# Kernel optimization log

Measured on AMD Instinct MI355X. Metric: run time of the kernel, lower is better.

## Reference

```python
import jax, jax.numpy as jnp
import numpy as np

B, S, HID = 1, 2048, 4096
N_HEADS, N_KV, HEAD_DIM = 32, 8, 128
N_REP = N_HEADS // N_KV
ROPE_THETA = 10000.0
NEG_INF = -1e9


def setup_inputs() -> dict:
    key = jax.random.key(0)
    ks = jax.random.split(key, 5)
    hidden_states = jax.random.normal(ks[0], (B, S, HID), dtype=jnp.float32)
    Wq = jax.random.normal(ks[1], (HID, N_HEADS * HEAD_DIM), dtype=jnp.float32) * 0.02
    Wk = jax.random.normal(ks[2], (HID, N_KV * HEAD_DIM), dtype=jnp.float32) * 0.02
    Wv = jax.random.normal(ks[3], (HID, N_KV * HEAD_DIM), dtype=jnp.float32) * 0.02
    Wo = jax.random.normal(ks[4], (N_HEADS * HEAD_DIM, HID), dtype=jnp.float32) * 0.02
    # causal additive mask [B, 1, S, S]
    causal = jnp.tril(jnp.ones((S, S), dtype=bool))
    attention_mask = jnp.where(causal, 0.0, NEG_INF).astype(jnp.float32)[None, None]
    position_ids = jnp.broadcast_to(jnp.arange(S, dtype=jnp.int32)[None], (B, S))
    return {
        "hidden_states": hidden_states, "Wq": Wq, "Wk": Wk, "Wv": Wv, "Wo": Wo,
        "attention_mask": attention_mask, "position_ids": position_ids,
    }


def _rotate_half(x):
    half = x.shape[-1] // 2
    return jnp.concatenate([-x[..., half:], x[..., :half]], axis=-1)


def _rope_tables(position_ids):
    # inv_freq: [head_dim/2]
    inv_freq = 1.0 / (ROPE_THETA ** (jnp.arange(0, HEAD_DIM, 2, dtype=jnp.float32) / HEAD_DIM))
    # freqs: [B, S, head_dim/2]
    freqs = position_ids.astype(jnp.float32)[..., None] * inv_freq
    emb = jnp.concatenate([freqs, freqs], axis=-1)  # [B, S, head_dim]
    # [B, 1, S, head_dim] to broadcast over heads
    return jnp.cos(emb)[:, None], jnp.sin(emb)[:, None]


def reference(hidden_states, Wq, Wk, Wv, Wo, attention_mask, position_ids):
    b, s, _ = hidden_states.shape
    # projections -> [B, H, S, D]
    q = (hidden_states @ Wq).reshape(b, s, N_HEADS, HEAD_DIM).transpose(0, 2, 1, 3)
    k = (hidden_states @ Wk).reshape(b, s, N_KV, HEAD_DIM).transpose(0, 2, 1, 3)
    v = (hidden_states @ Wv).reshape(b, s, N_KV, HEAD_DIM).transpose(0, 2, 1, 3)
    cos, sin = _rope_tables(position_ids)
    q = q * cos + _rotate_half(q) * sin
    k = k * cos + _rotate_half(k) * sin
    # GQA repeat_kv (repeat_interleave over head dim)
    k = jnp.repeat(k, N_REP, axis=1)
    v = jnp.repeat(v, N_REP, axis=1)
    scores = jnp.einsum("bhqd,bhkd->bhqk", q, k) / jnp.sqrt(jnp.float32(HEAD_DIM))
    scores = scores + attention_mask
    probs = jax.nn.softmax(scores.astype(jnp.float32), axis=-1).astype(q.dtype)
    attn = jnp.einsum("bhqk,bhkd->bhqd", probs, v)
    attn = attn.transpose(0, 2, 1, 3).reshape(b, s, N_HEADS * HEAD_DIM)
    return attn @ Wo
```

## Files before the change

kernel.cpp:

```cpp
#include <hip/hip_runtime.h>
#include <hip/hip_bf16.h>

#define S_LEN 2048
#define HIDDEN 4096
#define NH 32
#define NKV 8
#define HD 128
#define NQKV 6144

typedef __bf16 bf16_t;
typedef __bf16 bf16x8 __attribute__((ext_vector_type(8)));
typedef __bf16 bf16x4 __attribute__((ext_vector_type(4)));
typedef float f32x4 __attribute__((ext_vector_type(4)));

typedef __attribute__((address_space(1))) void gvoid;
typedef __attribute__((address_space(3))) void lvoid;

__device__ __forceinline__ void gload_lds16(const void* g, void* l) {
    __builtin_amdgcn_global_load_lds((gvoid*)g, (lvoid*)l, 16, 0, 0);
}

__device__ __forceinline__ float fast_exp2(float x) {
    return __builtin_amdgcn_exp2f(x);
}

__global__ void cast_bf16_kernel(const float* __restrict__ in, bf16_t* __restrict__ out, int n4) {
    int stride = gridDim.x * blockDim.x;
    for (int idx = blockIdx.x * blockDim.x + threadIdx.x; idx < n4; idx += stride) {
        float4 v = ((const float4*)in)[idx];
        bf16x4 o;
        o.x = (bf16_t)v.x; o.y = (bf16_t)v.y; o.z = (bf16_t)v.z; o.w = (bf16_t)v.w;
        ((bf16x4*)out)[idx] = o;
    }
}

__global__ __launch_bounds__(256) void transpose_cast_kernel(const float* __restrict__ in,
                                                             bf16_t* __restrict__ out,
                                                             int ldin, int ldout) {
    __shared__ float t[32][33];
    int c0 = blockIdx.x * 32, r0 = blockIdx.y * 32;
    int tx = threadIdx.x, ty = threadIdx.y;
#pragma unroll
    for (int i = 0; i < 4; ++i)
        t[ty + i * 8][tx] = in[(size_t)(r0 + ty + i * 8) * ldin + c0 + tx];
    __syncthreads();
#pragma unroll
    for (int i = 0; i < 4; ++i)
        out[(size_t)(c0 + ty + i * 8) * ldout + r0 + tx] = (bf16_t)t[tx][ty + i * 8];
}

__global__ __launch_bounds__(256) void transpose_bf16_kernel(const bf16_t* __restrict__ in,
                                                             bf16_t* __restrict__ out,
                                                             int ldin, int ldout) {
    __shared__ float t[32][33];
    int c0 = blockIdx.x * 32, r0 = blockIdx.y * 32;
    int tx = threadIdx.x, ty = threadIdx.y;
#pragma unroll
    for (int i = 0; i < 4; ++i)
        t[ty + i * 8][tx] = (float)in[(size_t)(r0 + ty + i * 8) * ldin + c0 + tx];
    __syncthreads();
#pragma unroll
    for (int i = 0; i < 4; ++i)
        out[(size_t)(c0 + ty + i * 8) * ldout + r0 + tx] = (bf16_t)t[tx][ty + i * 8];
}

template<typename OutT>
__global__ __launch_bounds__(512, 2) void gemm_ring_kernel(const bf16_t* __restrict__ A,
                                                           const bf16_t* __restrict__ Bt,
                                                           OutT* __restrict__ C,
                                                           int M, int N, int K) {
    __shared__ bf16_t As[3][128 * 32];
    __shared__ bf16_t Bs[3][256 * 32];
    const int tid = threadIdx.x;
    const int lane = tid & 63, w = tid >> 6;
    const int wm = w >> 2, wn = w & 3;
    const int g = lane >> 4, c16 = lane & 15;
    const int srow = lane >> 2;
    const int scg = ((lane & 3) ^ ((lane >> 3) & 3)) * 8;
    const int rdc = (g ^ ((c16 >> 1) & 3)) * 8;

    const int nbm = M / 128;
    const int cpx = gridDim.x >> 3;
    const int bid = blockIdx.x;
    const int swz = (bid & 7) * cpx + (bid >> 3);
    const int bm = swz % nbm, bn = swz / nbm;

    const bf16_t* Ab = A + (size_t)(bm * 128) * K;
    const bf16_t* Bb = Bt + (size_t)(bn * 256) * K;

    auto stage = [&](int slot, int kt) {
        const bf16_t* Ak = Ab + (size_t)kt * 32;
        const bf16_t* Bk = Bb + (size_t)kt * 32;
        {
            int rb = 16 * w;
            gload_lds16(Ak + (size_t)(rb + srow) * K + scg, &As[slot][rb * 32]);
        }
#pragma unroll
        for (int j = 0; j < 2; ++j) {
            int rb = 32 * w + 16 * j;
            gload_lds16(Bk + (size_t)(rb + srow) * K + scg, &Bs[slot][rb * 32]);
        }
    };

    f32x4 acc[4][4];
#pragma unroll
    for (int i = 0; i < 4; ++i)
#pragma unroll
        for (int j = 0; j < 4; ++j)
            acc[i][j] = (f32x4){0.f, 0.f, 0.f, 0.f};

    const int NT = K / 32;
    stage(0, 0);
    stage(1, 1);

    int slot = 0, slot2 = 2;
    for (int t = 0; t < NT; ++t) {
        asm volatile("s_waitcnt vmcnt(3)" ::: "memory");
        __builtin_amdgcn_s_barrier();
        __builtin_amdgcn_sched_barrier(0);
        __builtin_amdgcn_s_setprio(1);

        bf16x8 af[4], bf[4];
#pragma unroll
        for (int i = 0; i < 4; ++i) {
            int arow = wm * 64 + i * 16 + c16;
            af[i] = *(const bf16x8*)&As[slot][arow * 32 + rdc];
            int brow = wn * 64 + i * 16 + c16;
            bf[i] = *(const bf16x8*)&Bs[slot][brow * 32 + rdc];
        }
        int nk = t + 2;
        if (nk >= NT) nk -= NT;
        stage(slot2, nk);

#pragma unroll
        for (int i = 0; i < 4; ++i)
#pragma unroll
            for (int j = 0; j < 4; ++j)
                acc[i][j] = __builtin_amdgcn_mfma_f32_16x16x32_bf16(af[i], bf[j], acc[i][j], 0, 0, 0);
        __builtin_amdgcn_s_setprio(0);

        slot = (slot + 1) % 3;
        slot2 = (slot2 + 1) % 3;
    }

#pragma unroll
    for (int mi = 0; mi < 4; ++mi)
#pragma unroll
        for (int ni = 0; ni < 4; ++ni) {
            int col = bn * 256 + wn * 64 + ni * 16 + c16;
#pragma unroll
            for (int r = 0; r < 4; ++r) {
                int row = bm * 128 + wm * 64 + mi * 16 + g * 4 + r;
                C[(size_t)row * N + col] = (OutT)acc[mi][ni][r];
            }
        }
}

__global__ void rope_kernel(const bf16_t* __restrict__ in, bf16_t* __restrict__ out,
                            const int* __restrict__ pos, int H, int ld, float scale) {
    int idx = blockIdx.x * blockDim.x + threadIdx.x;
    int total = S_LEN * H * 64;
    if (idx >= total) return;
    int d = idx & 63;
    int h = (idx >> 6) % H;
    int s = idx / (64 * H);
    const bf16_t* base = in + (size_t)s * ld + h * HD;
    float x0 = (float)base[d], x1 = (float)base[d + 64];
    float p = (float)pos[s];
    float invf = fast_exp2(-0.20762050593046935f * (float)d);
    float f = p * invf;
    float sn, cs;
    __sincosf(f, &sn, &cs);
    float o0 = (x0 * cs - x1 * sn) * scale;
    float o1 = (x1 * cs + x0 * sn) * scale;
    bf16_t* ob = out + ((size_t)h * S_LEN + s) * HD;
    ob[d] = (bf16_t)o0;
    ob[d + 64] = (bf16_t)o1;
}

#define PLD 68
__global__ __launch_bounds__(512) void attn_kernel(const bf16_t* __restrict__ Q,
                                                   const bf16_t* __restrict__ K,
                                                   const bf16_t* __restrict__ Vt,
                                                   bf16_t* __restrict__ O) {
    __shared__ bf16_t Ks[2][64 * 128];
    __shared__ bf16_t Vs[2][128 * 64];
    __shared__ bf16_t Pl[8][16 * PLD];
    const int tid = threadIdx.x;
    const int lane = tid & 63, w = tid >> 6;
    const int bid = blockIdx.x;
    const int h = bid & 31;
    const int x = bid >> 5;
    const int wg = w >> 2, wi = w & 3;
    const int qtile = wg == 0 ? x : 15 - x;
    const int qb = qtile * 128 + wi * 32;
    const int kv = h >> 2;
    const int g = lane >> 4, c16 = lane & 15;
    const int c7 = c16 & 7;
    const bf16_t* Qh = Q + (size_t)h * S_LEN * HD;
    const bf16_t* Kh = K + (size_t)kv * S_LEN * HD;
    const bf16_t* Vh = Vt + (size_t)kv * HD * S_LEN;
    bf16_t* P = Pl[w];

    auto stage = [&](int buf, int kb) {
        bf16_t* Kd = Ks[buf];
        bf16_t* Vd = Vs[buf];
#pragma unroll
        for (int j = 0; j < 2; ++j) {
            int i = w * 2 + j;
            {
                int row = 4 * i + (lane >> 4);
                int sc = (lane & 15) ^ (row & 7);
                gload_lds16(Kh + (size_t)(kb + row) * HD + sc * 8, Kd + i * 512);
            }
            {
                int row = 8 * i + (lane >> 3);
                int sc = (lane & 7) ^ ((lane >> 3) & 7);
                gload_lds16(Vh + (size_t)row * S_LEN + kb + sc * 8, Vd + i * 512);
            }
        }
    };

    bf16x8 qf[2][4];
#pragma unroll
    for (int rg = 0; rg < 2; ++rg)
#pragma unroll
        for (int c = 0; c < 4; ++c)
            qf[rg][c] = *(const bf16x8*)(Qh + (size_t)(qb + rg * 16 + c16) * HD + c * 32 + g * 8);

    bf16x8 ones;
#pragma unroll
    for (int j = 0; j < 8; ++j) ones[j] = (bf16_t)1.0f;

    f32x4 acc_o[2][8];
#pragma unroll
    for (int rg = 0; rg < 2; ++rg)
#pragma unroll
        for (int dt = 0; dt < 8; ++dt) acc_o[rg][dt] = (f32x4){0.f, 0.f, 0.f, 0.f};
    f32x4 acc_l[2] = {(f32x4){0.f, 0.f, 0.f, 0.f}, (f32x4){0.f, 0.f, 0.f, 0.f}};
    float m[2][4];
#pragma unroll
    for (int rg = 0; rg < 2; ++rg)
#pragma unroll
        for (int r = 0; r < 4; ++r) m[rg][r] = -1e30f;

    const int nkt = 32 - 2 * x;
    stage(0, 0);
    __syncthreads();
    int cur = 0;

    bf16x8 pf[2][2];
    for (int kt = 0; kt < nkt; ++kt) {
        if (kt + 1 < nkt) stage(cur ^ 1, (kt + 1) * 64);
        const int kb = kt * 64;
        const bf16_t* Kb = Ks[cur];
        const bf16_t* Vb = Vs[cur];

        if (kb <= qb + 31) {
            const bool diag = (kb + 63 > qb);

            f32x4 sacc[2][4];
#pragma unroll
            for (int rg = 0; rg < 2; ++rg)
#pragma unroll
                for (int t = 0; t < 4; ++t) sacc[rg][t] = (f32x4){0.f, 0.f, 0.f, 0.f};
#pragma unroll
            for (int t = 0; t < 4; ++t) {
                const bf16_t* krow = Kb + (t * 16 + c16) * 128;
#pragma unroll
                for (int cc = 0; cc < 4; ++cc) {
                    bf16x8 kf = *(const bf16x8*)(krow + (((cc * 4 + g) ^ c7) * 8));
                    sacc[0][t] = __builtin_amdgcn_mfma_f32_16x16x32_bf16(qf[0][cc], kf, sacc[0][t], 0, 0, 0);
                    sacc[1][t] = __builtin_amdgcn_mfma_f32_16x16x32_bf16(qf[1][cc], kf, sacc[1][t], 0, 0, 0);
                }
            }
#pragma unroll
            for (int rg = 0; rg < 2; ++rg) {
                float p[4][4], mxr[4];
#pragma unroll
                for (int r = 0; r < 4; ++r) {
                    int qq = qb + rg * 16 + g * 4 + r;
#pragma unroll
                    for (int t = 0; t < 4; ++t) {
                        float sv = sacc[rg][t][r];
                        if (diag && (kb + t * 16 + c16 > qq)) sv = -1e30f;
                        p[t][r] = sv;
                    }
                    float mx = fmaxf(fmaxf(p[0][r], p[1][r]), fmaxf(p[2][r], p[3][r]));
                    mx = fmaxf(mx, __shfl_xor(mx, 1));
                    mx = fmaxf(mx, __shfl_xor(mx, 2));
                    mx = fmaxf(mx, __shfl_xor(mx, 4));
                    mx = fmaxf(mx, __shfl_xor(mx, 8));
                    mxr[r] = mx;
                }
                bool resc = false;
#pragma unroll
                for (int r = 0; r < 4; ++r) resc = resc || (mxr[r] > m[rg][r] + 8.f);
                if (__any(resc)) {
#pragma unroll
                    for (int r = 0; r < 4; ++r) {
                        float mn = fmaxf(m[rg][r], mxr[r]);
                        float al = fast_exp2(m[rg][r] - mn);
                        m[rg][r] = mn;
                        acc_l[rg][r] *= al;
#pragma unroll
                        for (int dt = 0; dt < 8; ++dt) acc_o[rg][dt][r] *= al;
                    }
                }
#pragma unroll
                for (int r = 0; r < 4; ++r)
#pragma unroll
                    for (int t = 0; t < 4; ++t)
                        p[t][r] = fast_exp2(p[t][r] - m[rg][r]);
#pragma unroll
                for (int t = 0; t < 4; ++t)
#pragma unroll
                    for (int r = 0; r < 4; ++r)
                        P[(g * 4 + r) * PLD + t * 16 + c16] = (bf16_t)p[t][r];
                pf[rg][0] = *(const bf16x8*)(P + c16 * PLD + g * 8);
                pf[rg][1] = *(const bf16x8*)(P + c16 * PLD + 32 + g * 8);
            }
            acc_l[0] = __builtin_amdgcn_mfma_f32_16x16x32_bf16(pf[0][0], ones, acc_l[0], 0, 0, 0);
            acc_l[0] = __builtin_amdgcn_mfma_f32_16x16x32_bf16(pf[0][1], ones, acc_l[0], 0, 0, 0);
            acc_l[1] = __builtin_amdgcn_mfma_f32_16x16x32_bf16(pf[1][0], ones, acc_l[1], 0, 0, 0);
            acc_l[1] = __builtin_amdgcn_mfma_f32_16x16x32_bf16(pf[1][1], ones, acc_l[1], 0, 0, 0);
#pragma unroll
            for (int dt = 0; dt < 8; ++dt) {
                const bf16_t* vrow = Vb + (dt * 16 + c16) * 64;
                bf16x8 vf0 = *(const bf16x8*)(vrow + ((g ^ c7) * 8));
                bf16x8 vf1 = *(const bf16x8*)(vrow + (((4 + g) ^ c7) * 8));
                acc_o[0][dt] = __builtin_amdgcn_mfma_f32_16x16x32_bf16(pf[0][0], vf0, acc_o[0][dt], 0, 0, 0);
                acc_o[0][dt] = __builtin_amdgcn_mfma_f32_16x16x32_bf16(pf[0][1], vf1, acc_o[0][dt], 0, 0, 0);
                acc_o[1][dt] = __builtin_amdgcn_mfma_f32_16x16x32_bf16(pf[1][0], vf0, acc_o[1][dt], 0, 0, 0);
                acc_o[1][dt] = __builtin_amdgcn_mfma_f32_16x16x32_bf16(pf[1][1], vf1, acc_o[1][dt], 0, 0, 0);
            }
        }
        __syncthreads();
        cur ^= 1;
    }
#pragma unroll
    for (int rg = 0; rg < 2; ++rg) {
        float inv_l[4];
#pragma unroll
        for (int r = 0; r < 4; ++r) inv_l[r] = 1.f / acc_l[rg][r];
#pragma unroll
        for (int dt = 0; dt < 8; ++dt)
#pragma unroll
            for (int r = 0; r < 4; ++r)
                O[(size_t)(qb + rg * 16 + g * 4 + r) * HIDDEN + h * HD + dt * 16 + c16] =
                    (bf16_t)(acc_o[rg][dt][r] * inv_l[r]);
    }
}

extern "C" void kernel_launch(void* const* d_in, const int* in_sizes, int n_in,
                              void* d_out, int out_size, void* d_ws, size_t ws_size,
                              hipStream_t stream) {
    const float* hs = (const float*)d_in[0];
    const float* Wq = (const float*)d_in[1];
    const float* Wk = (const float*)d_in[2];
    const float* Wv = (const float*)d_in[3];
    const float* Wo = (const float*)d_in[4];
    const int* pos = (const int*)d_in[6];
    float* out = (float*)d_out;

    char* ws = (char*)d_ws;
    size_t off = 0;
    auto alloc = [&](size_t bytes) -> void* {
        void* p = ws + off;
        off += (bytes + 255) & ~(size_t)255;
        return p;
    };
    bf16_t* hB    = (bf16_t*)alloc((size_t)S_LEN * HIDDEN * 2);
    bf16_t* WqkvT = (bf16_t*)alloc((size_t)NQKV * HIDDEN * 2);
    bf16_t* WoT   = (bf16_t*)alloc((size_t)HIDDEN * HIDDEN * 2);
    bf16_t* QKV   = (bf16_t*)alloc((size_t)S_LEN * NQKV * 2);
    bf16_t* Qr    = (bf16_t*)alloc((size_t)NH * S_LEN * HD * 2);
    bf16_t* Kr    = (bf16_t*)alloc((size_t)NKV * S_LEN * HD * 2);
    bf16_t* Vt    = (bf16_t*)alloc((size_t)NKV * HD * S_LEN * 2);
    bf16_t* Oat   = (bf16_t*)alloc((size_t)S_LEN * HIDDEN * 2);

    dim3 tb(32, 8);
    cast_bf16_kernel<<<2048, 256, 0, stream>>>(hs, hB, S_LEN * HIDDEN / 4);
    transpose_cast_kernel<<<dim3(HIDDEN / 32, HIDDEN / 32), tb, 0, stream>>>(Wq, WqkvT, HIDDEN, HIDDEN);
    transpose_cast_kernel<<<dim3(1024 / 32, HIDDEN / 32), tb, 0, stream>>>(Wk, WqkvT + (size_t)4096 * HIDDEN, 1024, HIDDEN);
    transpose_cast_kernel<<<dim3(1024 / 32, HIDDEN / 32), tb, 0, stream>>>(Wv, WqkvT + (size_t)5120 * HIDDEN, 1024, HIDDEN);
    transpose_cast_kernel<<<dim3(HIDDEN / 32, HIDDEN / 32), tb, 0, stream>>>(Wo, WoT, HIDDEN, HIDDEN);
    gemm_ring_kernel<bf16_t><<<(S_LEN / 128) * (NQKV / 256), 512, 0, stream>>>(hB, WqkvT, QKV, S_LEN, NQKV, HIDDEN);
    rope_kernel<<<(S_LEN * NH * 64 + 255) / 256, 256, 0, stream>>>(QKV, Qr, pos, NH, NQKV, 0.1275174310f);
    rope_kernel<<<(S_LEN * NKV * 64 + 255) / 256, 256, 0, stream>>>(QKV + 4096, Kr, pos, NKV, NQKV, 1.0f);
    transpose_bf16_kernel<<<dim3(1024 / 32, S_LEN / 32), tb, 0, stream>>>(QKV + 5120, Vt, NQKV, S_LEN);
    attn_kernel<<<256, 512, 0, stream>>>(Qr, Kr, Vt, Oat);
    gemm_ring_kernel<float><<<(S_LEN / 128) * (HIDDEN / 256), 512, 0, stream>>>(Oat, WoT, out, S_LEN, HIDDEN, HIDDEN);
}
```

Measured before the change: 374.8 us.

## Vectorize transposes with packed bf16 pairs and retile GEMMs for more blocks

Transpose kernels now handle 64x64 tiles with float4/bf16x4 loads, pack pairs of rows into 32-bit words in shared memory, and emit 16-byte stores, which cuts the number of narrow global accesses. The GEMM is templated on its N tile width. QKV uses 192-wide tiles (512 blocks instead of 384), and the output projection uses 128-wide tiles (512 blocks instead of 256), so load per-stage and vmcnt waits are adjusted. This aims to fill the GPU's compute units better, at the cost of less reuse per tile and more reloads of A.

```diff
diff --git a/kernel.cpp b/kernel.cpp
--- a/kernel.cpp
+++ b/kernel.cpp
@@ -22,6 +22,14 @@
 
 __device__ __forceinline__ float fast_exp2(float x) {
     return __builtin_amdgcn_exp2f(x);
+}
+
+__device__ __forceinline__ unsigned int pack2_bf16(float lo, float hi) {
+    bf16_t l = (bf16_t)lo, h = (bf16_t)hi;
+    unsigned short lu, hu;
+    __builtin_memcpy(&lu, &l, 2);
+    __builtin_memcpy(&hu, &h, 2);
+    return ((unsigned int)hu << 16) | (unsigned int)lu;
 }
 
 __global__ void cast_bf16_kernel(const float* __restrict__ in, bf16_t* __restrict__ out, int n4) {
@@ -37,40 +45,74 @@
 __global__ __launch_bounds__(256) void transpose_cast_kernel(const float* __restrict__ in,
                                                              bf16_t* __restrict__ out,
                                                              int ldin, int ldout) {
-    __shared__ float t[32][33];
-    int c0 = blockIdx.x * 32, r0 = blockIdx.y * 32;
-    int tx = threadIdx.x, ty = threadIdx.y;
-#pragma unroll
-    for (int i = 0; i < 4; ++i)
-        t[ty + i * 8][tx] = in[(size_t)(r0 + ty + i * 8) * ldin + c0 + tx];
+    __shared__ unsigned int t2[64][34];
+    const int c0 = blockIdx.x * 64, r0 = blockIdx.y * 64;
+    const int t = threadIdx.x;
+    const int tx4 = t & 15, tp = t >> 4;
+#pragma unroll
+    for (int i = 0; i < 2; ++i) {
+        int rp = tp + i * 16;
+        const float* p0 = &in[(size_t)(r0 + 2 * rp) * ldin + c0 + tx4 * 4];
+        float4 a = *(const float4*)p0;
+        float4 b = *(const float4*)(p0 + ldin);
+        t2[tx4 * 4 + 0][rp] = pack2_bf16(a.x, b.x);
+        t2[tx4 * 4 + 1][rp] = pack2_bf16(a.y, b.y);
+        t2[tx4 * 4 + 2][rp] = pack2_bf16(a.z, b.z);
+        t2[tx4 * 4 + 3][rp] = pack2_bf16(a.w, b.w);
+    }
     __syncthreads();
-#pragma unroll
-    for (int i = 0; i < 4; ++i)
-        out[(size_t)(c0 + ty + i * 8) * ldout + r0 + tx] = (bf16_t)t[tx][ty + i * 8];
+    const int q = t & 3, cc = t >> 2;
+    uint2 v0 = *(const uint2*)&t2[cc][q * 8 + 0];
+    uint2 v1 = *(const uint2*)&t2[cc][q * 8 + 2];
+    uint2 v2 = *(const uint2*)&t2[cc][q * 8 + 4];
+    uint2 v3 = *(const uint2*)&t2[cc][q * 8 + 6];
+    bf16_t* o = &out[(size_t)(c0 + cc) * ldout + r0 + q * 16];
+    *(uint4*)o = make_uint4(v0.x, v0.y, v1.x, v1.y);
+    *(uint4*)(o + 8) = make_uint4(v2.x, v2.y, v3.x, v3.y);
 }
 
 __global__ __launch_bounds__(256) void transpose_bf16_kernel(const bf16_t* __restrict__ in,
                                                              bf16_t* __restrict__ out,
                                                              int ldin, int ldout) {
-    __shared__ float t[32][33];
-    int c0 = blockIdx.x * 32, r0 = blockIdx.y * 32;
-    int tx = threadIdx.x, ty = threadIdx.y;
-#pragma unroll
-    for (int i = 0; i < 4; ++i)
-        t[ty + i * 8][tx] = (float)in[(size_t)(r0 + ty + i * 8) * ldin + c0 + tx];
+    __shared__ unsigned int t2[64][34];
+    const int c0 = blockIdx.x * 64, r0 = blockIdx.y * 64;
+    const int t = threadIdx.x;
+    const int tx4 = t & 15, tp = t >> 4;
+#pragma unroll
+    for (int i = 0; i < 2; ++i) {
+        int rp = tp + i * 16;
+        const bf16_t* p0 = &in[(size_t)(r0 + 2 * rp) * ldin + c0 + tx4 * 4];
+        bf16x4 a = *(const bf16x4*)p0;
+        bf16x4 b = *(const bf16x4*)(p0 + ldin);
+#pragma unroll
+        for (int k2 = 0; k2 < 4; ++k2) {
+            unsigned short lu, hu;
+            bf16_t la = a[k2], hb = b[k2];
+            __builtin_memcpy(&lu, &la, 2);
+            __builtin_memcpy(&hu, &hb, 2);
+            t2[tx4 * 4 + k2][rp] = ((unsigned int)hu << 16) | (unsigned int)lu;
+        }
+    }
     __syncthreads();
-#pragma unroll
-    for (int i = 0; i < 4; ++i)
-        out[(size_t)(c0 + ty + i * 8) * ldout + r0 + tx] = (bf16_t)t[tx][ty + i * 8];
-}
-
-template<typename OutT>
+    const int q = t & 3, cc = t >> 2;
+    uint2 v0 = *(const uint2*)&t2[cc][q * 8 + 0];
+    uint2 v1 = *(const uint2*)&t2[cc][q * 8 + 2];
+    uint2 v2 = *(const uint2*)&t2[cc][q * 8 + 4];
+    uint2 v3 = *(const uint2*)&t2[cc][q * 8 + 6];
+    bf16_t* o = &out[(size_t)(c0 + cc) * ldout + r0 + q * 16];
+    *(uint4*)o = make_uint4(v0.x, v0.y, v1.x, v1.y);
+    *(uint4*)(o + 8) = make_uint4(v2.x, v2.y, v3.x, v3.y);
+}
+
+template<int BN, typename OutT>
 __global__ __launch_bounds__(512, 2) void gemm_ring_kernel(const bf16_t* __restrict__ A,
                                                            const bf16_t* __restrict__ Bt,
                                                            OutT* __restrict__ C,
                                                            int M, int N, int K) {
+    constexpr int NF = BN / 64;
+    constexpr int VMN = (BN == 256) ? 3 : 2;
     __shared__ bf16_t As[3][128 * 32];
-    __shared__ bf16_t Bs[3][256 * 32];
+    __shared__ bf16_t Bs[3][BN * 32];
     const int tid = threadIdx.x;
     const int lane = tid & 63, w = tid >> 6;
     const int wm = w >> 2, wn = w & 3;
@@ -86,27 +128,45 @@
     const int bm = swz % nbm, bn = swz / nbm;
 
     const bf16_t* Ab = A + (size_t)(bm * 128) * K;
-    const bf16_t* Bb = Bt + (size_t)(bn * 256) * K;
+    const bf16_t* Bb = Bt + (size_t)bn * BN * K;
 
     auto stage = [&](int slot, int kt) {
         const bf16_t* Ak = Ab + (size_t)kt * 32;
         const bf16_t* Bk = Bb + (size_t)kt * 32;
-        {
+        if constexpr (BN == 256) {
             int rb = 16 * w;
             gload_lds16(Ak + (size_t)(rb + srow) * K + scg, &As[slot][rb * 32]);
-        }
-#pragma unroll
-        for (int j = 0; j < 2; ++j) {
-            int rb = 32 * w + 16 * j;
+#pragma unroll
+            for (int j = 0; j < 2; ++j) {
+                int rb2 = 32 * w + 16 * j;
+                gload_lds16(Bk + (size_t)(rb2 + srow) * K + scg, &Bs[slot][rb2 * 32]);
+            }
+        } else if constexpr (BN == 192) {
+            if (w < 4) {
+#pragma unroll
+                for (int j = 0; j < 3; ++j) {
+                    int rb = 48 * w + 16 * j;
+                    gload_lds16(Bk + (size_t)(rb + srow) * K + scg, &Bs[slot][rb * 32]);
+                }
+            } else {
+#pragma unroll
+                for (int j = 0; j < 2; ++j) {
+                    int rb = 32 * (w - 4) + 16 * j;
+                    gload_lds16(Ak + (size_t)(rb + srow) * K + scg, &As[slot][rb * 32]);
+                }
+            }
+        } else {
+            int rb = 16 * w;
+            gload_lds16(Ak + (size_t)(rb + srow) * K + scg, &As[slot][rb * 32]);
             gload_lds16(Bk + (size_t)(rb + srow) * K + scg, &Bs[slot][rb * 32]);
         }
     };
 
-    f32x4 acc[4][4];
+    f32x4 acc[4][NF];
 #pragma unroll
     for (int i = 0; i < 4; ++i)
 #pragma unroll
-        for (int j = 0; j < 4; ++j)
+        for (int j = 0; j < NF; ++j)
             acc[i][j] = (f32x4){0.f, 0.f, 0.f, 0.f};
 
     const int NT = K / 32;
@@ -115,18 +175,21 @@
 
     int slot = 0, slot2 = 2;
     for (int t = 0; t < NT; ++t) {
-        asm volatile("s_waitcnt vmcnt(3)" ::: "memory");
+        asm volatile("s_waitcnt vmcnt(%0)" :: "n"(VMN) : "memory");
         __builtin_amdgcn_s_barrier();
         __builtin_amdgcn_sched_barrier(0);
         __builtin_amdgcn_s_setprio(1);
 
-        bf16x8 af[4], bf[4];
+        bf16x8 af[4], bf[NF];
 #pragma unroll
         for (int i = 0; i < 4; ++i) {
             int arow = wm * 64 + i * 16 + c16;
             af[i] = *(const bf16x8*)&As[slot][arow * 32 + rdc];
-            int brow = wn * 64 + i * 16 + c16;
-            bf[i] = *(const bf16x8*)&Bs[slot][brow * 32 + rdc];
+        }
+#pragma unroll
+        for (int j = 0; j < NF; ++j) {
+            int brow = wn * (BN / 4) + j * 16 + c16;
+            bf[j] = *(const bf16x8*)&Bs[slot][brow * 32 + rdc];
         }
         int nk = t + 2;
         if (nk >= NT) nk -= NT;
@@ -135,7 +198,7 @@
 #pragma unroll
         for (int i = 0; i < 4; ++i)
 #pragma unroll
-            for (int j = 0; j < 4; ++j)
+            for (int j = 0; j < NF; ++j)
                 acc[i][j] = __builtin_amdgcn_mfma_f32_16x16x32_bf16(af[i], bf[j], acc[i][j], 0, 0, 0);
         __builtin_amdgcn_s_setprio(0);
 
@@ -146,8 +209,8 @@
 #pragma unroll
     for (int mi = 0; mi < 4; ++mi)
 #pragma unroll
-        for (int ni = 0; ni < 4; ++ni) {
-            int col = bn * 256 + wn * 64 + ni * 16 + c16;
+        for (int ni = 0; ni < NF; ++ni) {
+            int col = bn * BN + wn * (BN / 4) + ni * 16 + c16;
 #pragma unroll
             for (int r = 0; r < 4; ++r) {
                 int row = bm * 128 + wm * 64 + mi * 16 + g * 4 + r;
@@ -379,16 +442,15 @@
     bf16_t* Vt    = (bf16_t*)alloc((size_t)NKV * HD * S_LEN * 2);
     bf16_t* Oat   = (bf16_t*)alloc((size_t)S_LEN * HIDDEN * 2);
 
-    dim3 tb(32, 8);
     cast_bf16_kernel<<<2048, 256, 0, stream>>>(hs, hB, S_LEN * HIDDEN / 4);
-    transpose_cast_kernel<<<dim3(HIDDEN / 32, HIDDEN / 32), tb, 0, stream>>>(Wq, WqkvT, HIDDEN, HIDDEN);
-    transpose_cast_kernel<<<dim3(1024 / 32, HIDDEN / 32), tb, 0, stream>>>(Wk, WqkvT + (size_t)4096 * HIDDEN, 1024, HIDDEN);
-    transpose_cast_kernel<<<dim3(1024 / 32, HIDDEN / 32), tb, 0, stream>>>(Wv, WqkvT + (size_t)5120 * HIDDEN, 1024, HIDDEN);
-    transpose_cast_kernel<<<dim3(HIDDEN / 32, HIDDEN / 32), tb, 0, stream>>>(Wo, WoT, HIDDEN, HIDDEN);
-    gemm_ring_kernel<bf16_t><<<(S_LEN / 128) * (NQKV / 256), 512, 0, stream>>>(hB, WqkvT, QKV, S_LEN, NQKV, HIDDEN);
+    transpose_cast_kernel<<<dim3(HIDDEN / 64, HIDDEN / 64), 256, 0, stream>>>(Wq, WqkvT, HIDDEN, HIDDEN);
+    transpose_cast_kernel<<<dim3(1024 / 64, HIDDEN / 64), 256, 0, stream>>>(Wk, WqkvT + (size_t)4096 * HIDDEN, 1024, HIDDEN);
+    transpose_cast_kernel<<<dim3(1024 / 64, HIDDEN / 64), 256, 0, stream>>>(Wv, WqkvT + (size_t)5120 * HIDDEN, 1024, HIDDEN);
+    transpose_cast_kernel<<<dim3(HIDDEN / 64, HIDDEN / 64), 256, 0, stream>>>(Wo, WoT, HIDDEN, HIDDEN);
+    gemm_ring_kernel<192, bf16_t><<<(S_LEN / 128) * (NQKV / 192), 512, 0, stream>>>(hB, WqkvT, QKV, S_LEN, NQKV, HIDDEN);
     rope_kernel<<<(S_LEN * NH * 64 + 255) / 256, 256, 0, stream>>>(QKV, Qr, pos, NH, NQKV, 0.1275174310f);
     rope_kernel<<<(S_LEN * NKV * 64 + 255) / 256, 256, 0, stream>>>(QKV + 4096, Kr, pos, NKV, NQKV, 1.0f);
-    transpose_bf16_kernel<<<dim3(1024 / 32, S_LEN / 32), tb, 0, stream>>>(QKV + 5120, Vt, NQKV, S_LEN);
+    transpose_bf16_kernel<<<dim3(1024 / 64, S_LEN / 64), 256, 0, stream>>>(QKV + 5120, Vt, NQKV, S_LEN);
     attn_kernel<<<256, 512, 0, stream>>>(Qr, Kr, Vt, Oat);
-    gemm_ring_kernel<float><<<(S_LEN / 128) * (HIDDEN / 256), 512, 0, stream>>>(Oat, WoT, out, S_LEN, HIDDEN, HIDDEN);
-}
+    gemm_ring_kernel<128, float><<<(S_LEN / 128) * (HIDDEN / 128), 512, 0, stream>>>(Oat, WoT, out, S_LEN, HIDDEN, HIDDEN);
+}
```

After: 365.8 us. -2.4%, faster.
